# Optimization experiments

Hardware: AMD Instinct MI355X
Metric: run time of the kernel (lower is better)

The kernel has to match this reference:

```python
import jax, jax.numpy as jnp
import numpy as np

K_NEIGS = 3
M_PROB = 1.0
EPS = 1e-12


def _gen_G_single(ft):
    """Build normalized hypergraph Laplacian G [N,N] from node coords ft [N,3].

    Mirrors construct_H_with_KNN (is_probH=True, m_prob=1) + generate_G_from_H
    from the HGNN reference code: per-center KNN hyperedges with probabilistic
    incidence exp(-d^2/(m_prob*avg_d)^2), then G = Dv^-1/2 H De^-1 H^T Dv^-1/2.
    """
    N = ft.shape[0]
    # squared pairwise Euclidean distances [N,N]
    sq_norm = jnp.sum(ft * ft, axis=1)
    sq = jnp.maximum(sq_norm[:, None] + sq_norm[None, :] - 2.0 * ft @ ft.T, 0.0)
    dist = jnp.sqrt(sq + EPS)
    avg_dis = jnp.mean(dist, axis=1)  # per-center mean distance [N]
    # K nearest neighbors per center (self is always included: sq[c,c]=0)
    neg_sq, idx = jax.lax.top_k(-sq, K_NEIGS)  # [N,K]
    # prob incidence: exp(-d^2 / (m_prob*avg)^2); neg_sq = -d^2
    vals = jnp.exp(neg_sq / (M_PROB * avg_dis[:, None]) ** 2)  # [N,K]
    # H[node, edge]: column c holds the K neighbors of center c
    H = jnp.zeros((N, N), ft.dtype).at[idx, jnp.arange(N)[:, None]].set(vals)
    de = jnp.sum(H, axis=0)              # edge degrees [N]
    dv = jnp.sum(H, axis=1)              # vertex degrees [N]
    inv_de = 1.0 / de
    dv2 = dv ** -0.5
    HW = H * inv_de[None, :]
    G = (dv2[:, None] * (HW @ H.T)) * dv2[None, :]
    return G


def reference(x, W1, b1, Wc, bc):
    # gen_G: per-batch hypergraph G [B,N,N]
    G = jax.vmap(_gen_G_single)(x)
    # HGNN_conv with both args = G: out = G @ (G @ W1 + b1)  -> [B,N,H1]
    f = jnp.matmul(G, jnp.matmul(G, W1) + b1)
    # max-pool over nodes, then classifier
    f = jnp.max(f, axis=1)               # [B,H1]
    return f @ Wc + bc                   # [B,class_num]


def setup_inputs() -> dict:
    key = jax.random.key(0)
    k1, k2, k3, k4, k5 = jax.random.split(key, 5)
    B, N, H1, C = 4, 2048, 128, 8
    x = jax.random.normal(k1, (B, N, 3), dtype=jnp.float32)
    W1 = jax.random.normal(k2, (N, H1), dtype=jnp.float32) / np.sqrt(N)
    b1 = jax.random.normal(k3, (H1,), dtype=jnp.float32) * 0.01
    Wc = jax.random.normal(k4, (H1, C), dtype=jnp.float32) / np.sqrt(H1)
    bc = jax.random.normal(k5, (C,), dtype=jnp.float32) * 0.01
    return {"x": x, "W1": W1, "b1": b1, "Wc": Wc, "bc": bc}
```

## Files before the change

### kernel.cpp

```cpp
#include <hip/hip_runtime.h>
#include <math.h>

#define NN 2048
#define BB 4
#define HD 128
#define CNUM 8
#define WPB 4
#define PCHUNK 64
#define NCHUNKS (NN / PCHUNK)

typedef unsigned long long u64;

__device__ __forceinline__ u64 pack_key(float sq, int j) {
    return ((u64)__float_as_uint(sq) << 32) | (unsigned)j;
}
__device__ __forceinline__ void ins3(u64 k, u64& k0, u64& k1, u64& k2) {
    u64 a = k  < k2 ? k  : k2;
    u64 b = k0 > a  ? k0 : a;
    k0    = k0 < a  ? k0 : a;
    k2    = k1 > b  ? k1 : b;
    k1    = k1 < b  ? k1 : b;
}

__global__ __launch_bounds__(256) void k_dist(
        const float* __restrict__ x,
        int* __restrict__ idx, float* __restrict__ vals,
        float* __restrict__ de, float* __restrict__ dv) {
    __shared__ float4 sp[NN];
    const int b = blockIdx.y;
    const float* xb = x + (size_t)b * NN * 3;
    for (int q = threadIdx.x; q < NN; q += 256) {
        const float a = xb[3 * q], c = xb[3 * q + 1], d = xb[3 * q + 2];
        sp[q] = make_float4(a, c, d, a * a + c * c + d * d);
    }
    __syncthreads();

    const int wave = threadIdx.x >> 6;
    const int lane = threadIdx.x & 63;
    const int i = blockIdx.x * WPB + wave;
    const float4 ci = sp[i];
    u64 k0 = ~0ull, k1 = ~0ull, k2 = ~0ull;
    float dsA = 0.f, dsB = 0.f;
    for (int t = lane; t < NN; t += 256) {
        const float4 pa = sp[t];
        const float4 pv = sp[t + 64];
        const float4 pc = sp[t + 128];
        const float4 pd = sp[t + 192];
        const float qa = fmaxf(ci.w + pa.w - 2.0f * (ci.x * pa.x + ci.y * pa.y + ci.z * pa.z), 0.0f);
        const float qb = fmaxf(ci.w + pv.w - 2.0f * (ci.x * pv.x + ci.y * pv.y + ci.z * pv.z), 0.0f);
        const float qc = fmaxf(ci.w + pc.w - 2.0f * (ci.x * pc.x + ci.y * pc.y + ci.z * pc.z), 0.0f);
        const float qd = fmaxf(ci.w + pd.w - 2.0f * (ci.x * pd.x + ci.y * pd.y + ci.z * pd.z), 0.0f);
        dsA += __builtin_amdgcn_sqrtf(qa + 1e-12f) + __builtin_amdgcn_sqrtf(qc + 1e-12f);
        dsB += __builtin_amdgcn_sqrtf(qb + 1e-12f) + __builtin_amdgcn_sqrtf(qd + 1e-12f);
        ins3(pack_key(qa, t),       k0, k1, k2);
        ins3(pack_key(qb, t + 64),  k0, k1, k2);
        ins3(pack_key(qc, t + 128), k0, k1, k2);
        ins3(pack_key(qd, t + 192), k0, k1, k2);
    }
    float dsum = dsA + dsB;
    for (int off = 32; off > 0; off >>= 1) {
        const u64 o0 = __shfl_xor(k0, off);
        const u64 o1 = __shfl_xor(k1, off);
        const u64 o2 = __shfl_xor(k2, off);
        dsum += __shfl_xor(dsum, off);
        ins3(o0, k0, k1, k2);
        ins3(o1, k0, k1, k2);
        ins3(o2, k0, k1, k2);
    }
    if (lane == 0) {
        const float s0 = __uint_as_float((unsigned)(k0 >> 32));
        const float s1 = __uint_as_float((unsigned)(k1 >> 32));
        const float s2 = __uint_as_float((unsigned)(k2 >> 32));
        const int   i0 = (int)(k0 & 0xffffffffu);
        const int   i1 = (int)(k1 & 0xffffffffu);
        const int   i2 = (int)(k2 & 0xffffffffu);
        const float avg = dsum * (1.0f / NN);
        const float inva2 = 1.0f / (avg * avg);
        const float v0 = expf(-s0 * inva2);
        const float v1 = expf(-s1 * inva2);
        const float v2 = expf(-s2 * inva2);
        const int base = (b * NN + i) * 3;
        idx[base] = i0; idx[base + 1] = i1; idx[base + 2] = i2;
        vals[base] = v0; vals[base + 1] = v1; vals[base + 2] = v2;
        de[b * NN + i] = v0 + v1 + v2;
        atomicAdd(&dv[b * NN + i0], v0);
        atomicAdd(&dv[b * NN + i1], v1);
        atomicAdd(&dv[b * NN + i2], v2);
    }
}

__global__ void k_conv1(const float* __restrict__ W1, const int* __restrict__ idx,
                        const float* __restrict__ vals, const float* __restrict__ de,
                        const float* __restrict__ dv, float* __restrict__ Z1) {
    const int e = blockIdx.x * 2 + (threadIdx.x >> 7);
    const int b = blockIdx.y, h = threadIdx.x & (HD - 1);
    const int base = (b * NN + e) * 3;
    const int j0 = idx[base], j1 = idx[base + 1], j2 = idx[base + 2];
    const float v0 = vals[base], v1 = vals[base + 1], v2 = vals[base + 2];
    const float ide = 1.0f / de[b * NN + e];
    const float g0 = v0 * rsqrtf(dv[b * NN + j0]);
    const float g1 = v1 * rsqrtf(dv[b * NN + j1]);
    const float g2 = v2 * rsqrtf(dv[b * NN + j2]);
    const float y = ide * (g0 * W1[j0 * HD + h] + g1 * W1[j1 * HD + h] + g2 * W1[j2 * HD + h]);
    atomicAdd(&Z1[((size_t)(b * NN + j0)) * HD + h], v0 * y);
    atomicAdd(&Z1[((size_t)(b * NN + j1)) * HD + h], v1 * y);
    atomicAdd(&Z1[((size_t)(b * NN + j2)) * HD + h], v2 * y);
}

__global__ void k_conv2(const float* __restrict__ b1, const int* __restrict__ idx,
                        const float* __restrict__ vals, const float* __restrict__ de,
                        const float* __restrict__ dv, const float* __restrict__ Z1,
                        float* __restrict__ Z2) {
    const int e = blockIdx.x * 2 + (threadIdx.x >> 7);
    const int b = blockIdx.y, h = threadIdx.x & (HD - 1);
    const int base = (b * NN + e) * 3;
    const int j0 = idx[base], j1 = idx[base + 1], j2 = idx[base + 2];
    const float v0 = vals[base], v1 = vals[base + 1], v2 = vals[base + 2];
    const float ide = 1.0f / de[b * NN + e];
    const float bh = b1[h];
    const float d0 = rsqrtf(dv[b * NN + j0]);
    const float d1 = rsqrtf(dv[b * NN + j1]);
    const float d2 = rsqrtf(dv[b * NN + j2]);
    const float f0 = d0 * Z1[((size_t)(b * NN + j0)) * HD + h] + bh;
    const float f1 = d1 * Z1[((size_t)(b * NN + j1)) * HD + h] + bh;
    const float f2 = d2 * Z1[((size_t)(b * NN + j2)) * HD + h] + bh;
    const float y = ide * (v0 * d0 * f0 + v1 * d1 * f1 + v2 * d2 * f2);
    atomicAdd(&Z2[((size_t)(b * NN + j0)) * HD + h], v0 * y);
    atomicAdd(&Z2[((size_t)(b * NN + j1)) * HD + h], v1 * y);
    atomicAdd(&Z2[((size_t)(b * NN + j2)) * HD + h], v2 * y);
}

__global__ void k_pool1(const float* __restrict__ dv, const float* __restrict__ Z2,
                        float* __restrict__ pmax) {
    const int b = blockIdx.x, ch = blockIdx.y, h = threadIdx.x;
    const int v0 = ch * PCHUNK;
    float mx = -INFINITY;
    for (int v = v0; v < v0 + PCHUNK; ++v) {
        const float d2 = rsqrtf(dv[b * NN + v]);
        mx = fmaxf(mx, d2 * Z2[((size_t)(b * NN + v)) * HD + h]);
    }
    pmax[(b * NCHUNKS + ch) * HD + h] = mx;
}

__global__ void k_pool2(const float* __restrict__ Wc, const float* __restrict__ bc,
                        const float* __restrict__ pmax, float* __restrict__ out) {
    __shared__ float smax[HD];
    const int b = blockIdx.x, h = threadIdx.x;
    float mx = -INFINITY;
    for (int c = 0; c < NCHUNKS; ++c)
        mx = fmaxf(mx, pmax[(b * NCHUNKS + c) * HD + h]);
    smax[h] = mx;
    __syncthreads();
    if (h < CNUM) {
        float acc = bc[h];
        for (int q = 0; q < HD; ++q) acc += smax[q] * Wc[q * CNUM + h];
        out[b * CNUM + h] = acc;
    }
}

extern "C" void kernel_launch(void* const* d_in, const int* in_sizes, int n_in,
                              void* d_out, int out_size, void* d_ws, size_t ws_size,
                              hipStream_t stream) {
    const float* x  = (const float*)d_in[0];
    const float* W1 = (const float*)d_in[1];
    const float* b1 = (const float*)d_in[2];
    const float* Wc = (const float*)d_in[3];
    const float* bc = (const float*)d_in[4];
    float* out = (float*)d_out;

    float* ws = (float*)d_ws;
    float* dv   = ws;
    float* Z1   = dv + BB * NN;
    float* Z2   = Z1 + (size_t)BB * NN * HD;
    float* vals = Z2 + (size_t)BB * NN * HD;
    float* de   = vals + BB * NN * 3;
    int*   idx  = (int*)(de + BB * NN);
    float* pmax = (float*)(idx + BB * NN * 3);

    hipMemsetAsync(dv, 0, (size_t)(BB * NN) * (1 + 2 * HD) * sizeof(float), stream);

    k_dist<<<dim3(NN / WPB, BB), 256, 0, stream>>>(x, idx, vals, de, dv);
    k_conv1<<<dim3(NN / 2, BB), 256, 0, stream>>>(W1, idx, vals, de, dv, Z1);
    k_conv2<<<dim3(NN / 2, BB), 256, 0, stream>>>(b1, idx, vals, de, dv, Z1, Z2);
    k_pool1<<<dim3(BB, NCHUNKS), HD, 0, stream>>>(dv, Z2, pmax);
    k_pool2<<<BB, HD, 0, stream>>>(Wc, bc, pmax, out);
}
```

Baseline: 120.6 us.

## Fold Z1/Z2 zeroing into k_dist, fuse pooling kernels, simplify KNN wave merge

The large memset that cleared the Z1/Z2 accumulators is removed. Each k_dist thread now zeroes one float4 of that region, and only the small dv, pool-max and counter area is still memset. The two pooling kernels become one: each block does an atomicMax on an order-preserving uint encoding, and the last block to finish, detected with an atomic counter, runs the classifier. The per-wave top-3 merge now uses three successive wave-min reductions with pop-front instead of shuffling and inserting all three keys at every step. The aim is to cut a memset pass over the 8MB buffer, one kernel launch and some shuffle work, at the cost of extra global stores in k_dist and atomic contention in the pool kernel.

```diff
diff --git a/kernel.cpp b/kernel.cpp
--- a/kernel.cpp
+++ b/kernel.cpp
@@ -8,6 +8,7 @@
 #define WPB 4
 #define PCHUNK 64
 #define NCHUNKS (NN / PCHUNK)
+#define NPOOLB (BB * NCHUNKS)
 
 typedef unsigned long long u64;
 
@@ -21,12 +22,23 @@
     k2    = k1 > b  ? k1 : b;
     k1    = k1 < b  ? k1 : b;
 }
+__device__ __forceinline__ u64 wave_min_u64(u64 m) {
+    for (int off = 32; off > 0; off >>= 1) {
+        const u64 o = __shfl_xor(m, off);
+        m = o < m ? o : m;
+    }
+    return m;
+}
 
 __global__ __launch_bounds__(256) void k_dist(
         const float* __restrict__ x,
         int* __restrict__ idx, float* __restrict__ vals,
-        float* __restrict__ de, float* __restrict__ dv) {
+        float* __restrict__ de, float* __restrict__ dv,
+        float4* __restrict__ zv4) {
     __shared__ float4 sp[NN];
+    const int zi = (blockIdx.y * gridDim.x + blockIdx.x) * 256 + threadIdx.x;
+    zv4[zi] = make_float4(0.f, 0.f, 0.f, 0.f);
+
     const int b = blockIdx.y;
     const float* xb = x + (size_t)b * NN * 3;
     for (int q = threadIdx.x; q < NN; q += 256) {
@@ -58,22 +70,25 @@
         ins3(pack_key(qd, t + 192), k0, k1, k2);
     }
     float dsum = dsA + dsB;
-    for (int off = 32; off > 0; off >>= 1) {
-        const u64 o0 = __shfl_xor(k0, off);
-        const u64 o1 = __shfl_xor(k1, off);
-        const u64 o2 = __shfl_xor(k2, off);
+    for (int off = 32; off > 0; off >>= 1)
         dsum += __shfl_xor(dsum, off);
-        ins3(o0, k0, k1, k2);
-        ins3(o1, k0, k1, k2);
-        ins3(o2, k0, k1, k2);
+    u64 m0, m1, m2;
+    {
+        m0 = wave_min_u64(k0);
+        bool e = (k0 == m0);
+        k0 = e ? k1 : k0;  k1 = e ? k2 : k1;  k2 = e ? ~0ull : k2;
+        m1 = wave_min_u64(k0);
+        e = (k0 == m1);
+        k0 = e ? k1 : k0;
+        m2 = wave_min_u64(k0);
     }
     if (lane == 0) {
-        const float s0 = __uint_as_float((unsigned)(k0 >> 32));
-        const float s1 = __uint_as_float((unsigned)(k1 >> 32));
-        const float s2 = __uint_as_float((unsigned)(k2 >> 32));
-        const int   i0 = (int)(k0 & 0xffffffffu);
-        const int   i1 = (int)(k1 & 0xffffffffu);
-        const int   i2 = (int)(k2 & 0xffffffffu);
+        const float s0 = __uint_as_float((unsigned)(m0 >> 32));
+        const float s1 = __uint_as_float((unsigned)(m1 >> 32));
+        const float s2 = __uint_as_float((unsigned)(m2 >> 32));
+        const int   i0 = (int)(m0 & 0xffffffffu);
+        const int   i1 = (int)(m1 & 0xffffffffu);
+        const int   i2 = (int)(m2 & 0xffffffffu);
         const float avg = dsum * (1.0f / NN);
         const float inva2 = 1.0f / (avg * avg);
         const float v0 = expf(-s0 * inva2);
@@ -130,8 +145,11 @@
     atomicAdd(&Z2[((size_t)(b * NN + j2)) * HD + h], v2 * y);
 }
 
-__global__ void k_pool1(const float* __restrict__ dv, const float* __restrict__ Z2,
-                        float* __restrict__ pmax) {
+__global__ void k_pool(const float* __restrict__ dv, const float* __restrict__ Z2,
+                       const float* __restrict__ Wc, const float* __restrict__ bc,
+                       unsigned* __restrict__ pmaxK, unsigned* __restrict__ done,
+                       float* __restrict__ out) {
+    __shared__ bool last;
     const int b = blockIdx.x, ch = blockIdx.y, h = threadIdx.x;
     const int v0 = ch * PCHUNK;
     float mx = -INFINITY;
@@ -139,22 +157,25 @@
         const float d2 = rsqrtf(dv[b * NN + v]);
         mx = fmaxf(mx, d2 * Z2[((size_t)(b * NN + v)) * HD + h]);
     }
-    pmax[(b * NCHUNKS + ch) * HD + h] = mx;
-}
-
-__global__ void k_pool2(const float* __restrict__ Wc, const float* __restrict__ bc,
-                        const float* __restrict__ pmax, float* __restrict__ out) {
-    __shared__ float smax[HD];
-    const int b = blockIdx.x, h = threadIdx.x;
-    float mx = -INFINITY;
-    for (int c = 0; c < NCHUNKS; ++c)
-        mx = fmaxf(mx, pmax[(b * NCHUNKS + c) * HD + h]);
-    smax[h] = mx;
+    unsigned u = __float_as_uint(mx);
+    u = (u & 0x80000000u) ? ~u : (u | 0x80000000u);
+    atomicMax(&pmaxK[b * HD + h], u);
+    __threadfence();
+    if (threadIdx.x == 0)
+        last = (atomicAdd(done, 1u) == NPOOLB - 1);
     __syncthreads();
-    if (h < CNUM) {
-        float acc = bc[h];
-        for (int q = 0; q < HD; ++q) acc += smax[q] * Wc[q * CNUM + h];
-        out[b * CNUM + h] = acc;
+    if (last) {
+        __threadfence();
+        if (threadIdx.x < BB * CNUM) {
+            const int ob = threadIdx.x >> 3, c = threadIdx.x & (CNUM - 1);
+            float acc = bc[c];
+            for (int q = 0; q < HD; ++q) {
+                unsigned w = pmaxK[ob * HD + q];
+                w = (w & 0x80000000u) ? (w ^ 0x80000000u) : ~w;
+                acc += __uint_as_float(w) * Wc[q * CNUM + c];
+            }
+            out[ob * CNUM + c] = acc;
+        }
     }
 }
 
@@ -168,20 +189,21 @@
     const float* bc = (const float*)d_in[4];
     float* out = (float*)d_out;
 
-    float* ws = (float*)d_ws;
-    float* dv   = ws;
-    float* Z1   = dv + BB * NN;
-    float* Z2   = Z1 + (size_t)BB * NN * HD;
-    float* vals = Z2 + (size_t)BB * NN * HD;
-    float* de   = vals + BB * NN * 3;
-    int*   idx  = (int*)(de + BB * NN);
-    float* pmax = (float*)(idx + BB * NN * 3);
-
-    hipMemsetAsync(dv, 0, (size_t)(BB * NN) * (1 + 2 * HD) * sizeof(float), stream);
-
-    k_dist<<<dim3(NN / WPB, BB), 256, 0, stream>>>(x, idx, vals, de, dv);
+    float*    ws    = (float*)d_ws;
+    float*    dv    = ws;
+    unsigned* pmaxK = (unsigned*)(dv + BB * NN);
+    unsigned* done  = pmaxK + BB * HD;
+    float*    Z1    = (float*)(done + 4);
+    float*    Z2    = Z1 + (size_t)BB * NN * HD;
+    float*    vals  = Z2 + (size_t)BB * NN * HD;
+    float*    de    = vals + BB * NN * 3;
+    int*      idx   = (int*)(de + BB * NN);
+    float4*   zv4   = (float4*)Z1;
+
+    hipMemsetAsync(dv, 0, (size_t)(BB * NN + BB * HD + 4) * sizeof(float), stream);
+
+    k_dist <<<dim3(NN / WPB, BB), 256, 0, stream>>>(x, idx, vals, de, dv, zv4);
     k_conv1<<<dim3(NN / 2, BB), 256, 0, stream>>>(W1, idx, vals, de, dv, Z1);
     k_conv2<<<dim3(NN / 2, BB), 256, 0, stream>>>(b1, idx, vals, de, dv, Z1, Z2);
-    k_pool1<<<dim3(BB, NCHUNKS), HD, 0, stream>>>(dv, Z2, pmax);
-    k_pool2<<<BB, HD, 0, stream>>>(Wc, bc, pmax, out);
-}
+    k_pool <<<dim3(BB, NCHUNKS), HD, 0, stream>>>(dv, Z2, Wc, bc, pmaxK, done, out);
+}
```

Result: slower. 128.1 us (+6.2%).
